# Kernel tuning notes

Measured on AMD Instinct MI355X. Metric: run time of the kernel, lower is better.

The kernel has to match this reference:

```python
import jax, jax.numpy as jnp
import numpy as np

HDIM = 1024
N_CLASSES = 50257
CUTOFFS = [2000, 10000, N_CLASSES]  # shortlist=2000, clusters: [2000,10000), [10000,50257)
DIV = 4.0
HEAD_SIZE = CUTOFFS[0] + 2  # shortlist + 2 cluster logits


def setup_inputs() -> dict:
    key = jax.random.key(0)
    ks = jax.random.split(key, 12)
    B, S, K = 8, 512, 256
    N = B * K
    hsz0 = int(HDIM // (DIV ** 1))  # 256
    hsz1 = int(HDIM // (DIV ** 2))  # 64
    osz0 = CUTOFFS[1] - CUTOFFS[0]  # 8000
    osz1 = CUTOFFS[2] - CUTOFFS[1]  # 40257
    w = 0.02
    return {
        "targets": jax.random.randint(ks[0], (N,), 0, N_CLASSES),
        "last_hidden_states": jax.random.normal(ks[1], (B, S, HDIM), dtype=jnp.float32),
        "cls_tokens_batch": jax.random.normal(ks[2], (B, HDIM), dtype=jnp.float32),
        "idx": jax.random.randint(ks[3], (B, K), 0, S),
        "head_W": jax.random.normal(ks[4], (HEAD_SIZE, HDIM), dtype=jnp.float32) * w,
        "head_b": jnp.zeros((HEAD_SIZE,), dtype=jnp.float32),
        "proj0_W": jax.random.normal(ks[5], (hsz0, HDIM), dtype=jnp.float32) * w,
        "out0_W": jax.random.normal(ks[6], (osz0, hsz0), dtype=jnp.float32) * w,
        "proj1_W": jax.random.normal(ks[7], (hsz1, HDIM), dtype=jnp.float32) * w,
        "out1_W": jax.random.normal(ks[8], (osz1, hsz1), dtype=jnp.float32) * w,
    }


def reference(targets, last_hidden_states, cls_tokens_batch, idx,
              head_W, head_b, proj0_W, out0_W, proj1_W, out1_W):
    # Gather context token embeddings: [B, K, H] -> [N, H]
    B, S, H = last_hidden_states.shape
    x = last_hidden_states[jnp.arange(B)[:, None], idx].reshape(-1, H)
    N = x.shape[0]
    c0, c1 = CUTOFFS[0], CUTOFFS[1]

    # Head: shortlist logits + per-cluster routing logits, [N, c0+2]
    head_logprob = jax.nn.log_softmax(x @ head_W.T + head_b, axis=-1)
    # Tail clusters: low-rank projection then output GEMM + log-softmax
    lp0 = jax.nn.log_softmax((x @ proj0_W.T) @ out0_W.T, axis=-1)  # [N, 8000]
    lp1 = jax.nn.log_softmax((x @ proj1_W.T) @ out1_W.T, axis=-1)  # [N, 40257]

    n = jnp.arange(N)
    t = targets
    short = head_logprob[n, jnp.clip(t, 0, c0 - 1)]
    mid = head_logprob[:, c0] + lp0[n, jnp.clip(t - c0, 0, lp0.shape[1] - 1)]
    high = head_logprob[:, c0 + 1] + lp1[n, jnp.clip(t - c1, 0, lp1.shape[1] - 1)]
    out = jnp.where(t < c0, short, jnp.where(t < c1, mid, high))  # target log-probs [N]
    loss = -jnp.mean(out)
    return out, loss
```

## Files before the change

### kernel.cpp

```cpp
#include <hip/hip_runtime.h>
#include <hip/hip_bf16.h>

#define NROWS 2048
#define L2E 1.4426950408889634f

typedef float f32x4 __attribute__((ext_vector_type(4)));
typedef __bf16 bf16x8 __attribute__((ext_vector_type(8)));
typedef short s16x8 __attribute__((ext_vector_type(8)));

typedef const __attribute__((address_space(1))) unsigned int* gas_t;
typedef __attribute__((address_space(3))) unsigned int* las_t;

__device__ __forceinline__ unsigned short f2bf(float f) {
    unsigned int u = __float_as_uint(f);
    unsigned int r = (u + 0x7FFFu + ((u >> 16) & 1u)) >> 16;
    return (unsigned short)r;
}
__device__ __forceinline__ float bf2f(unsigned short u) {
    return __uint_as_float((unsigned int)u << 16);
}
__device__ __forceinline__ f32x4 mfma16(s16x8 a, s16x8 b, f32x4 c) {
    return __builtin_amdgcn_mfma_f32_16x16x32_bf16(
        __builtin_bit_cast(bf16x8, a), __builtin_bit_cast(bf16x8, b), c, 0, 0, 0);
}

__global__ void k_prologue(const float* __restrict__ lhs, const int* __restrict__ idx,
                           const float* __restrict__ hw, const float* __restrict__ p0w,
                           const float* __restrict__ p1w, const float* __restrict__ o0w,
                           const float* __restrict__ o1w, const float* __restrict__ hb,
                           const int* __restrict__ tgt,
                           unsigned short* __restrict__ xb, unsigned short* __restrict__ hWb,
                           unsigned short* __restrict__ pW01, unsigned short* __restrict__ o0Wb,
                           unsigned short* __restrict__ o1Wb,
                           float* __restrict__ bias_s, int* __restrict__ tc) {
    int bid = blockIdx.x;
    if (bid < 2048) {
        int tid = bid * 256 + threadIdx.x;
        int n = tid >> 8;
        int c = (tid & 255) << 2;
        int b = n >> 8, k = n & 255;
        int srow = idx[(b << 8) + k];
        const float4 v = *reinterpret_cast<const float4*>(
            lhs + (((size_t)b << 9) + srow) * 1024 + c);
        ushort4 o = make_ushort4(f2bf(v.x), f2bf(v.y), f2bf(v.z), f2bf(v.w));
        *reinterpret_cast<ushort4*>(xb + (size_t)n * 1024 + c) = o;
        return;
    }
    bid -= 2048;
    if (bid < 6968) {
        const long B0 = 2048L * 1024;
        const long B1 = B0 + 384L * 1024;
        const long B2 = B1 + 8064L * 256;
        const long B3 = B2 + 40320L * 64;
        long e = ((long)bid * 256 + threadIdx.x) * 4;
        if (e >= B3) return;
        const float* src; unsigned short* dst; long rows; int colshift; long base;
        float sc;
        if (e < B0)      { base = 0;  src = hw;  dst = hWb;  rows = 2002;  colshift = 10; sc = L2E; }
        else if (e < B1) {
            long l = e - B0;
            long row = l >> 10;
            unsigned short* d = pW01 + l;
            ushort4 o;
            if (row < 256) {
                float4 v = *reinterpret_cast<const float4*>(p0w + l);
                o = make_ushort4(f2bf(v.x), f2bf(v.y), f2bf(v.z), f2bf(v.w));
            } else if (row < 320) {
                float4 v = *reinterpret_cast<const float4*>(p1w + (l - 256L * 1024));
                o = make_ushort4(f2bf(v.x), f2bf(v.y), f2bf(v.z), f2bf(v.w));
            } else {
                o = make_ushort4(0, 0, 0, 0);
            }
            *reinterpret_cast<ushort4*>(d) = o;
            return;
        }
        else if (e < B2) { base = B1; src = o0w; dst = o0Wb; rows = 8000;  colshift = 8; sc = L2E; }
        else             { base = B2; src = o1w; dst = o1Wb; rows = 40257; colshift = 6; sc = L2E; }
        long l = e - base;
        long row = l >> colshift;
        ushort4 o;
        if (row < rows) {
            float4 v = *reinterpret_cast<const float4*>(src + l);
            o = make_ushort4(f2bf(v.x * sc), f2bf(v.y * sc), f2bf(v.z * sc), f2bf(v.w * sc));
        } else {
            o = make_ushort4(0, 0, 0, 0);
        }
        *reinterpret_cast<ushort4*>(dst + l) = o;
        return;
    }
    bid -= 6968;
    int n = bid * 256 + threadIdx.x;
    if (n >= 2048) return;
    bias_s[n] = (n < 2002) ? hb[n] * L2E : -1e30f;
    int t = tgt[n];
    tc[n] = min(t, 1999);
    tc[2048 + n] = min(max(t - 2000, 0), 7999);
    tc[4096 + n] = min(max(t - 10000, 0), 40256);
}

template <int NT>
__global__ __launch_bounds__(256)
void k_mm(const unsigned short* __restrict__ A, int lda,
          const unsigned short* __restrict__ B, int ldb,
          const float* __restrict__ bias, float* __restrict__ partial,
          unsigned short* __restrict__ hout, int hstride, int hcols, int fsplit) {
    __shared__ unsigned short As[2][128 * 64];
    __shared__ unsigned short Bs[2][128 * 64];
    const int tid = threadIdx.x;
    const int lane = tid & 63, wid = tid >> 6;
    const int wr = wid >> 1, wc = wid & 1;
    const int g = lane >> 4, cl = lane & 15;
    const int row0 = blockIdx.x * 128;
    const int col0 = blockIdx.y * 128;

    const int sr = wid * 8 + (lane >> 3);
    const int swz = ((lane & 7) ^ (lane >> 3)) * 8;
    const unsigned short* Ab = A + (size_t)(row0 + sr) * lda + swz;
    const unsigned short* Bb = B + (size_t)(col0 + sr) * ldb + swz;

    auto stage = [&](int buf, int kt) {
        const unsigned short* ga = Ab + kt;
        const unsigned short* gb = Bb + kt;
        unsigned short* la = &As[buf][wid * 8 * 64];
        unsigned short* lb = &Bs[buf][wid * 8 * 64];
#pragma unroll
        for (int i = 0; i < 4; ++i) {
            __builtin_amdgcn_global_load_lds((gas_t)(const void*)(ga + (size_t)i * 32 * lda),
                                             (las_t)(void*)(la + i * 32 * 64), 16, 0, 0);
            __builtin_amdgcn_global_load_lds((gas_t)(const void*)(gb + (size_t)i * 32 * ldb),
                                             (las_t)(void*)(lb + i * 32 * 64), 16, 0, 0);
        }
    };

    f32x4 acc[4][4] = {};
    stage(0, 0);
    asm volatile("s_waitcnt vmcnt(0)" ::: "memory");
    __builtin_amdgcn_s_barrier();
    const int sA = (cl & 7);
    for (int t = 0; t < NT; ++t) {
        if (t + 1 < NT) stage((t + 1) & 1, (t + 1) * 64);
        const unsigned short* Al = &As[t & 1][(wr * 64 + cl) * 64];
        const unsigned short* Bl = &Bs[t & 1][(wc * 64 + cl) * 64];
#pragma unroll
        for (int kk2 = 0; kk2 < 2; ++kk2) {
            const int slot = ((kk2 * 4 + g) ^ sA) * 8;
            s16x8 a[4], b[4];
#pragma unroll
            for (int mi = 0; mi < 4; ++mi)
                a[mi] = *reinterpret_cast<const s16x8*>(Al + mi * 16 * 64 + slot);
#pragma unroll
            for (int ni = 0; ni < 4; ++ni)
                b[ni] = *reinterpret_cast<const s16x8*>(Bl + ni * 16 * 64 + slot);
#pragma unroll
            for (int mi = 0; mi < 4; ++mi)
#pragma unroll
                for (int ni = 0; ni < 4; ++ni)
                    acc[mi][ni] = mfma16(a[mi], b[ni], acc[mi][ni]);
        }
        if (t + 1 < NT) {
            asm volatile("s_waitcnt vmcnt(0)" ::: "memory");
            __builtin_amdgcn_s_barrier();
        }
    }

    if ((int)blockIdx.y >= fsplit) {
        int c0 = col0 - fsplit * 128;
#pragma unroll
        for (int mi = 0; mi < 4; ++mi)
#pragma unroll
            for (int ni = 0; ni < 4; ++ni) {
                int col = c0 + wc * 64 + ni * 16 + cl;
                if (col < hcols) {
#pragma unroll
                    for (int r = 0; r < 4; ++r) {
                        int row = row0 + wr * 64 + mi * 16 + g * 4 + r;
                        hout[(size_t)row * hstride + col] = f2bf(acc[mi][ni][r]);
                    }
                }
            }
    } else {
        float bv[4];
#pragma unroll
        for (int ni = 0; ni < 4; ++ni)
            bv[ni] = bias ? bias[col0 + wc * 64 + ni * 16 + cl] : 0.f;
        int strip = blockIdx.y * 2 + wc;
#pragma unroll
        for (int mi = 0; mi < 4; ++mi)
#pragma unroll
            for (int r = 0; r < 4; ++r) {
                float s = 0.f;
#pragma unroll
                for (int ni = 0; ni < 4; ++ni)
                    s += __builtin_amdgcn_exp2f(acc[mi][ni][r] + bv[ni]);
                s += __shfl_xor(s, 1, 64);
                s += __shfl_xor(s, 2, 64);
                s += __shfl_xor(s, 4, 64);
                s += __shfl_xor(s, 8, 64);
                if (cl == 0)
                    partial[(size_t)strip * NROWS + row0 + wr * 64 + mi * 16 + g * 4 + r] = s;
            }
    }
}

#define OUT1_IT 5
__global__ __launch_bounds__(256)
void k_tail(const unsigned short* __restrict__ h01, const unsigned short* __restrict__ o0Wb,
            const unsigned short* __restrict__ o1Wb, const unsigned short* __restrict__ xb,
            const float* __restrict__ headW, const float* __restrict__ hb,
            const float* __restrict__ o0w, const float* __restrict__ o1w,
            const int* __restrict__ tc,
            float* __restrict__ p0, float* __restrict__ p1,
            float* __restrict__ tgh, float* __restrict__ r0, float* __restrict__ r1,
            float* __restrict__ tg0, float* __restrict__ tg1) {
    __shared__ unsigned short smem[4][128 * 64];
    const int tid = threadIdx.x;
    const int lane = tid & 63, wid = tid >> 6;
    const int wr = wid >> 1, wc = wid & 1;
    const int g = lane >> 4, cl = lane & 15;
    int bid = blockIdx.x;

    if (bid < 1008) {
        const int row0 = (bid & 15) * 128;
        const int col0 = (bid >> 4) * 128;
        const int sr = wid * 8 + (lane >> 3);
        const int swz = ((lane & 7) ^ (lane >> 3)) * 8;
        const unsigned short* Ab = h01 + (size_t)(row0 + sr) * 320 + swz;
        const unsigned short* Bb = o0Wb + (size_t)(col0 + sr) * 256 + swz;
        auto stage = [&](int buf, int kt) {
            const unsigned short* ga = Ab + kt;
            const unsigned short* gb = Bb + kt;
            unsigned short* la = &smem[buf][wid * 8 * 64];
            unsigned short* lb = &smem[2 + buf][wid * 8 * 64];
#pragma unroll
            for (int i = 0; i < 4; ++i) {
                __builtin_amdgcn_global_load_lds((gas_t)(const void*)(ga + (size_t)i * 32 * 320),
                                                 (las_t)(void*)(la + i * 32 * 64), 16, 0, 0);
                __builtin_amdgcn_global_load_lds((gas_t)(const void*)(gb + (size_t)i * 32 * 256),
                                                 (las_t)(void*)(lb + i * 32 * 64), 16, 0, 0);
            }
        };
        f32x4 acc[4][4] = {};
        stage(0, 0);
        asm volatile("s_waitcnt vmcnt(0)" ::: "memory");
        __builtin_amdgcn_s_barrier();
        const int sA = (cl & 7);
        for (int t = 0; t < 4; ++t) {
            if (t < 3) stage((t + 1) & 1, (t + 1) * 64);
            const unsigned short* Al = &smem[t & 1][(wr * 64 + cl) * 64];
            const unsigned short* Bl = &smem[2 + (t & 1)][(wc * 64 + cl) * 64];
#pragma unroll
            for (int kk2 = 0; kk2 < 2; ++kk2) {
                const int slot = ((kk2 * 4 + g) ^ sA) * 8;
                s16x8 a[4], b[4];
#pragma unroll
                for (int mi = 0; mi < 4; ++mi)
                    a[mi] = *reinterpret_cast<const s16x8*>(Al + mi * 16 * 64 + slot);
#pragma unroll
                for (int ni = 0; ni < 4; ++ni)
                    b[ni] = *reinterpret_cast<const s16x8*>(Bl + ni * 16 * 64 + slot);
#pragma unroll
                for (int mi = 0; mi < 4; ++mi)
#pragma unroll
                    for (int ni = 0; ni < 4; ++ni)
                        acc[mi][ni] = mfma16(a[mi], b[ni], acc[mi][ni]);
            }
            if (t < 3) {
                asm volatile("s_waitcnt vmcnt(0)" ::: "memory");
                __builtin_amdgcn_s_barrier();
            }
        }
        int strip = (bid >> 4) * 2 + wc;
#pragma unroll
        for (int mi = 0; mi < 4; ++mi)
#pragma unroll
            for (int r = 0; r < 4; ++r) {
                float s = 0.f;
#pragma unroll
                for (int ni = 0; ni < 4; ++ni)
                    s += __builtin_amdgcn_exp2f(acc[mi][ni][r]);
                s += __shfl_xor(s, 1, 64);
                s += __shfl_xor(s, 2, 64);
                s += __shfl_xor(s, 4, 64);
                s += __shfl_xor(s, 8, 64);
                if (cl == 0)
                    p0[(size_t)strip * NROWS + row0 + wr * 64 + mi * 16 + g * 4 + r] = s;
            }
        return;
    }
    if (bid < 2016) {
        bid -= 1008;
        const int row0 = (bid & 15) * 128 + wr * 64;
        const int yb = bid >> 4;
        const int t0 = yb * OUT1_IT;
        s16x8 a[4][2];
#pragma unroll
        for (int mi = 0; mi < 4; ++mi)
#pragma unroll
            for (int kk = 0; kk < 2; ++kk)
                a[mi][kk] = *reinterpret_cast<const s16x8*>(
                    h01 + (size_t)(row0 + mi * 16 + cl) * 320 + 256 + kk * 32 + g * 8);
        const int sr = wid * 8 + (lane >> 3);
        const int swz = ((lane & 7) ^ (lane >> 3)) * 8;
        auto stage = [&](int buf, int tile) {
            const unsigned short* gb = o1Wb + ((size_t)tile * 128 + sr) * 64 + swz;
            unsigned short* lb = &smem[buf][wid * 8 * 64];
#pragma unroll
            for (int i = 0; i < 4; ++i)
                __builtin_amdgcn_global_load_lds((gas_t)(const void*)(gb + (size_t)i * 32 * 64),
                                                 (las_t)(void*)(lb + i * 32 * 64), 16, 0, 0);
        };
        float sexp[4][4] = {};
        const f32x4 z4 = {0.f, 0.f, 0.f, 0.f};
        stage(0, t0);
        asm volatile("s_waitcnt vmcnt(0)" ::: "memory");
        __builtin_amdgcn_s_barrier();
        int buf = 0;
        const int sA = (cl & 7);
#pragma unroll 1
        for (int it = 0; it < OUT1_IT; ++it) {
            if (it + 1 < OUT1_IT) stage(buf ^ 1, t0 + it + 1);
            const unsigned short* Bl = smem[buf];
#pragma unroll
            for (int ni = 0; ni < 4; ++ni) {
                const unsigned short* br = Bl + (wc * 64 + ni * 16 + cl) * 64;
                s16x8 b0 = *reinterpret_cast<const s16x8*>(br + (g ^ sA) * 8);
                s16x8 b1 = *reinterpret_cast<const s16x8*>(br + ((4 + g) ^ sA) * 8);
                f32x4 acc[4];
#pragma unroll
                for (int mi = 0; mi < 4; ++mi)
                    acc[mi] = mfma16(a[mi][0], b0, z4);
#pragma unroll
                for (int mi = 0; mi < 4; ++mi)
                    acc[mi] = mfma16(a[mi][1], b1, acc[mi]);
#pragma unroll
                for (int mi = 0; mi < 4; ++mi)
#pragma unroll
                    for (int r = 0; r < 4; ++r)
                        sexp[mi][r] += __builtin_amdgcn_exp2f(acc[mi][r]);
            }
            if (it + 1 < OUT1_IT) {
                asm volatile("s_waitcnt vmcnt(0)" ::: "memory");
                __builtin_amdgcn_s_barrier();
                buf ^= 1;
            }
        }
#pragma unroll
        for (int mi = 0; mi < 4; ++mi)
#pragma unroll
            for (int r = 0; r < 4; ++r) {
                float s = sexp[mi][r];
                s += __shfl_xor(s, 1, 64);
                s += __shfl_xor(s, 2, 64);
                s += __shfl_xor(s, 4, 64);
                s += __shfl_xor(s, 8, 64);
                if (cl == 0)
                    p1[(size_t)(yb * 2 + wc) * NROWS + row0 + mi * 16 + g * 4 + r] = s;
            }
        return;
    }
    bid -= 2016;
    int n = (bid * 256 + tid) >> 6;
    int tch = tc[n], tc0 = tc[2048 + n], tc1 = tc[4096 + n];
    const unsigned short* xr = xb + (size_t)n * 1024 + lane * 16;
    s16x8 x0 = *reinterpret_cast<const s16x8*>(xr);
    s16x8 x1 = *reinterpret_cast<const s16x8*>(xr + 8);
    const float* wh = headW + (size_t)tch * 1024 + lane * 16;
    const float* wa = headW + (size_t)2000 * 1024 + lane * 16;
    const float* wb = headW + (size_t)2001 * 1024 + lane * 16;
    float dh = 0.f, da = 0.f, db = 0.f;
#pragma unroll
    for (int i = 0; i < 8; ++i) {
        float xv = bf2f((unsigned short)x0[i]);
        dh += xv * wh[i]; da += xv * wa[i]; db += xv * wb[i];
    }
#pragma unroll
    for (int i = 0; i < 8; ++i) {
        float xv = bf2f((unsigned short)x1[i]);
        dh += xv * wh[8 + i]; da += xv * wa[8 + i]; db += xv * wb[8 + i];
    }
    ushort4 h0v = *reinterpret_cast<const ushort4*>(h01 + (size_t)n * 320 + lane * 4);
    float4 w0v = *reinterpret_cast<const float4*>(o0w + (size_t)tc0 * 256 + lane * 4);
    float d2 = bf2f(h0v.x) * w0v.x + bf2f(h0v.y) * w0v.y +
               bf2f(h0v.z) * w0v.z + bf2f(h0v.w) * w0v.w;
    float d3 = bf2f(h01[(size_t)n * 320 + 256 + lane]) * o1w[(size_t)tc1 * 64 + lane];
#pragma unroll
    for (int m = 1; m < 64; m <<= 1) {
        dh += __shfl_xor(dh, m, 64);
        da += __shfl_xor(da, m, 64);
        db += __shfl_xor(db, m, 64);
        d2 += __shfl_xor(d2, m, 64);
        d3 += __shfl_xor(d3, m, 64);
    }
    if (lane == 0) {
        tgh[n] = dh + hb[tch];
        r0[n] = da + hb[2000];
        r1[n] = db + hb[2001];
        tg0[n] = d2;
        tg1[n] = d3;
    }
}

__global__ void k_finalize(const float* __restrict__ ph, const float* __restrict__ p0,
                           const float* __restrict__ p1, const float* __restrict__ tgh,
                           const float* __restrict__ r0, const float* __restrict__ r1,
                           const float* __restrict__ tg0, const float* __restrict__ tg1,
                           const int* __restrict__ tgt, float* __restrict__ outv,
                           float* __restrict__ bsum) {
    int n = blockIdx.x * 128 + threadIdx.x;
    float sh = 0.f, s0 = 0.f, s1 = 0.f;
    for (int s = 0; s < 32; ++s) sh += ph[(size_t)s * NROWS + n];
    for (int s = 0; s < 126; ++s) s0 += p0[(size_t)s * NROWS + n];
    for (int s = 0; s < 126; ++s) s1 += p1[(size_t)s * NROWS + n];
    s0 -= 64.f;
    s1 -= 63.f;
    float lh = __logf(sh), l0 = __logf(s0), l1 = __logf(s1);
    int t = tgt[n];
    float o;
    if (t < 2000) o = tgh[n] - lh;
    else if (t < 10000) o = (r0[n] - lh) + (tg0[n] - l0);
    else o = (r1[n] - lh) + (tg1[n] - l1);
    outv[n] = o;
    __shared__ float red[128];
    red[threadIdx.x] = o;
    __syncthreads();
    for (int s = 64; s > 0; s >>= 1) {
        if (threadIdx.x < s) red[threadIdx.x] += red[threadIdx.x + s];
        __syncthreads();
    }
    if (threadIdx.x == 0) bsum[blockIdx.x] = red[0];
}

__global__ void k_loss(const float* __restrict__ bsum, float* __restrict__ loss) {
    float s = 0.f;
    for (int i = 0; i < 16; ++i) s += bsum[i];
    *loss = -s / (float)NROWS;
}

extern "C" void kernel_launch(void* const* d_in, const int* in_sizes, int n_in,
                              void* d_out, int out_size, void* d_ws, size_t ws_size,
                              hipStream_t stream) {
    const int* targets   = (const int*)d_in[0];
    const float* lhs     = (const float*)d_in[1];
    const int* idx       = (const int*)d_in[3];
    const float* head_W  = (const float*)d_in[4];
    const float* head_b  = (const float*)d_in[5];
    const float* proj0_W = (const float*)d_in[6];
    const float* out0_W  = (const float*)d_in[7];
    const float* proj1_W = (const float*)d_in[8];
    const float* out1_W  = (const float*)d_in[9];

    char* ws = (char*)d_ws;
    size_t off = 0;
    auto alloc = [&](size_t bytes) -> void* {
        void* p = ws + off;
        off += (bytes + 255) & ~(size_t)255;
        return p;
    };

    unsigned short* xb   = (unsigned short*)alloc((size_t)2048 * 1024 * 2);
    unsigned short* wB   = (unsigned short*)alloc((size_t)2432 * 1024 * 2);
    unsigned short* hWb  = wB;
    unsigned short* pW01 = wB + (size_t)2048 * 1024;
    unsigned short* o0Wb = (unsigned short*)alloc((size_t)8064 * 256 * 2);
    unsigned short* o1Wb = (unsigned short*)alloc((size_t)40320 * 64 * 2);
    unsigned short* h01  = (unsigned short*)alloc((size_t)2048 * 320 * 2);
    float* ph  = (float*)alloc((size_t)32 * 2048 * 4);
    float* p0  = (float*)alloc((size_t)126 * 2048 * 4);
    float* p1  = (float*)alloc((size_t)126 * 2048 * 4);
    float* tgh = (float*)alloc(2048 * 4);
    float* r0  = (float*)alloc(2048 * 4);
    float* r1  = (float*)alloc(2048 * 4);
    float* tg0 = (float*)alloc(2048 * 4);
    float* tg1 = (float*)alloc(2048 * 4);
    int*   tc  = (int*)alloc(3 * 2048 * 4);
    float* bias_s = (float*)alloc(2048 * 4);
    float* bsum = (float*)alloc(16 * 4);

    k_prologue<<<9024, 256, 0, stream>>>(lhs, idx, head_W, proj0_W, proj1_W, out0_W, out1_W,
                                         head_b, targets,
                                         xb, hWb, pW01, o0Wb, o1Wb, bias_s, tc);

    k_mm<16><<<dim3(16, 19), 256, 0, stream>>>(
        xb, 1024, wB, 1024, bias_s, ph, h01, 320, 320, 16);

    k_tail<<<2528, 256, 0, stream>>>(h01, o0Wb, o1Wb, xb, head_W, head_b, out0_W, out1_W,
                                     tc, p0, p1, tgh, r0, r1, tg0, tg1);

    float* outv = (float*)d_out;
    float* loss = (float*)d_out + NROWS;
    k_finalize<<<16, 128, 0, stream>>>(ph, p0, p1, tgh, r0, r1, tg0, tg1, targets, outv, bsum);
    k_loss<<<1, 1, 0, stream>>>(bsum, loss);
}
```

Baseline: 87.53 us.

## Compact rows by target cluster and skip tail GEMM tiles for absent rows

The prologue now builds per-cluster compacted row lists with a block-wide prefix scan over targets, recording the row count for each tail cluster. The tail GEMMs gather A rows through these lists and exit early for row tiles beyond the count, so only rows whose target falls in a cluster get that cluster's log-softmax denominator computed. Finalize reads the partial sums through the inverse index. With uniform random targets about 16% and 80% of rows land in the two clusters, so cluster 0 work shrinks a lot. The cost is a single-block serial scan in the prologue and indirect row loads.

```diff
diff --git a/kernel.cpp b/kernel.cpp
--- a/kernel.cpp
+++ b/kernel.cpp
@@ -32,7 +32,10 @@
                            unsigned short* __restrict__ xb, unsigned short* __restrict__ hWb,
                            unsigned short* __restrict__ pW01, unsigned short* __restrict__ o0Wb,
                            unsigned short* __restrict__ o1Wb,
-                           float* __restrict__ bias_s, int* __restrict__ tc) {
+                           float* __restrict__ bias_s, int* __restrict__ tc,
+                           int* __restrict__ rows0, int* __restrict__ rows1,
+                           int* __restrict__ idx0, int* __restrict__ idx1,
+                           int* __restrict__ cnt) {
     int bid = blockIdx.x;
     if (bid < 2048) {
         int tid = bid * 256 + threadIdx.x;
@@ -88,14 +91,42 @@
         *reinterpret_cast<ushort4*>(dst + l) = o;
         return;
     }
-    bid -= 6968;
-    int n = bid * 256 + threadIdx.x;
-    if (n >= 2048) return;
-    bias_s[n] = (n < 2002) ? hb[n] * L2E : -1e30f;
-    int t = tgt[n];
-    tc[n] = min(t, 1999);
-    tc[2048 + n] = min(max(t - 2000, 0), 7999);
-    tc[4096 + n] = min(max(t - 10000, 0), 40256);
+    __shared__ int sc0[256], sc1[256];
+    int t = threadIdx.x;
+    int myt[8];
+    int c0l = 0, c1l = 0;
+#pragma unroll
+    for (int i = 0; i < 8; ++i) {
+        int n = t * 8 + i;
+        int tt = tgt[n];
+        myt[i] = tt;
+        bias_s[n] = (n < 2002) ? hb[n] * L2E : -1e30f;
+        tc[n] = min(tt, 1999);
+        tc[2048 + n] = min(max(tt - 2000, 0), 7999);
+        tc[4096 + n] = min(max(tt - 10000, 0), 40256);
+        c0l += (tt >= 2000 && tt < 10000);
+        c1l += (tt >= 10000);
+    }
+    sc0[t] = c0l; sc1[t] = c1l;
+    __syncthreads();
+    for (int off = 1; off < 256; off <<= 1) {
+        int v0 = (t >= off) ? sc0[t - off] : 0;
+        int v1 = (t >= off) ? sc1[t - off] : 0;
+        __syncthreads();
+        sc0[t] += v0; sc1[t] += v1;
+        __syncthreads();
+    }
+    int p0pos = sc0[t] - c0l, p1pos = sc1[t] - c1l;
+#pragma unroll
+    for (int i = 0; i < 8; ++i) {
+        int n = t * 8 + i;
+        int tt = myt[i];
+        if (tt >= 2000 && tt < 10000) { rows0[p0pos] = n; idx0[n] = p0pos; ++p0pos; }
+        else idx0[n] = -1;
+        if (tt >= 10000) { rows1[p1pos] = n; idx1[n] = p1pos; ++p1pos; }
+        else idx1[n] = -1;
+    }
+    if (t == 255) { cnt[0] = sc0[255]; cnt[1] = sc1[255]; }
 }
 
 template <int NT>
@@ -209,6 +240,8 @@
             const float* __restrict__ headW, const float* __restrict__ hb,
             const float* __restrict__ o0w, const float* __restrict__ o1w,
             const int* __restrict__ tc,
+            const int* __restrict__ rows0, const int* __restrict__ rows1,
+            const int* __restrict__ cnt,
             float* __restrict__ p0, float* __restrict__ p1,
             float* __restrict__ tgh, float* __restrict__ r0, float* __restrict__ r1,
             float* __restrict__ tg0, float* __restrict__ tg1) {
@@ -220,22 +253,28 @@
     int bid = blockIdx.x;
 
     if (bid < 1008) {
-        const int row0 = (bid & 15) * 128;
+        const int c0n = cnt[0];
+        const int rt = bid & 15;
+        const int row0 = rt * 128;
+        if (row0 >= c0n) return;
         const int col0 = (bid >> 4) * 128;
         const int sr = wid * 8 + (lane >> 3);
         const int swz = ((lane & 7) ^ (lane >> 3)) * 8;
-        const unsigned short* Ab = h01 + (size_t)(row0 + sr) * 320 + swz;
+        const unsigned short* Arow[4];
+#pragma unroll
+        for (int i = 0; i < 4; ++i) {
+            int rp = min(row0 + sr + i * 32, c0n - 1);
+            Arow[i] = h01 + (size_t)rows0[rp] * 320 + swz;
+        }
         const unsigned short* Bb = o0Wb + (size_t)(col0 + sr) * 256 + swz;
         auto stage = [&](int buf, int kt) {
-            const unsigned short* ga = Ab + kt;
-            const unsigned short* gb = Bb + kt;
             unsigned short* la = &smem[buf][wid * 8 * 64];
             unsigned short* lb = &smem[2 + buf][wid * 8 * 64];
 #pragma unroll
             for (int i = 0; i < 4; ++i) {
-                __builtin_amdgcn_global_load_lds((gas_t)(const void*)(ga + (size_t)i * 32 * 320),
+                __builtin_amdgcn_global_load_lds((gas_t)(const void*)(Arow[i] + kt),
                                                  (las_t)(void*)(la + i * 32 * 64), 16, 0, 0);
-                __builtin_amdgcn_global_load_lds((gas_t)(const void*)(gb + (size_t)i * 32 * 256),
+                __builtin_amdgcn_global_load_lds((gas_t)(const void*)(Bb + kt + (size_t)i * 32 * 256),
                                                  (las_t)(void*)(lb + i * 32 * 64), 16, 0, 0);
             }
         };
@@ -289,16 +328,23 @@
     }
     if (bid < 2016) {
         bid -= 1008;
-        const int row0 = (bid & 15) * 128 + wr * 64;
+        const int c1n = cnt[1];
+        const int rt = bid & 15;
+        if (rt * 128 >= c1n) return;
+        const int row0c = rt * 128 + wr * 64;
         const int yb = bid >> 4;
         const int t0 = yb * OUT1_IT;
+        int grow[4];
+#pragma unroll
+        for (int mi = 0; mi < 4; ++mi)
+            grow[mi] = rows1[min(row0c + mi * 16 + cl, c1n - 1)];
         s16x8 a[4][2];
 #pragma unroll
         for (int mi = 0; mi < 4; ++mi)
 #pragma unroll
             for (int kk = 0; kk < 2; ++kk)
                 a[mi][kk] = *reinterpret_cast<const s16x8*>(
-                    h01 + (size_t)(row0 + mi * 16 + cl) * 320 + 256 + kk * 32 + g * 8);
+                    h01 + (size_t)grow[mi] * 320 + 256 + kk * 32 + g * 8);
         const int sr = wid * 8 + (lane >> 3);
         const int swz = ((lane & 7) ^ (lane >> 3)) * 8;
         auto stage = [&](int buf, int tile) {
@@ -354,7 +400,7 @@
                 s += __shfl_xor(s, 4, 64);
                 s += __shfl_xor(s, 8, 64);
                 if (cl == 0)
-                    p1[(size_t)(yb * 2 + wc) * NROWS + row0 + mi * 16 + g * 4 + r] = s;
+                    p1[(size_t)(yb * 2 + wc) * NROWS + row0c + mi * 16 + g * 4 + r] = s;
             }
         return;
     }
@@ -404,21 +450,30 @@
                            const float* __restrict__ p1, const float* __restrict__ tgh,
                            const float* __restrict__ r0, const float* __restrict__ r1,
                            const float* __restrict__ tg0, const float* __restrict__ tg1,
-                           const int* __restrict__ tgt, float* __restrict__ outv,
-                           float* __restrict__ bsum) {
+                           const int* __restrict__ tgt,
+                           const int* __restrict__ idx0, const int* __restrict__ idx1,
+                           float* __restrict__ outv, float* __restrict__ bsum) {
     int n = blockIdx.x * 128 + threadIdx.x;
-    float sh = 0.f, s0 = 0.f, s1 = 0.f;
+    float sh = 0.f;
     for (int s = 0; s < 32; ++s) sh += ph[(size_t)s * NROWS + n];
-    for (int s = 0; s < 126; ++s) s0 += p0[(size_t)s * NROWS + n];
-    for (int s = 0; s < 126; ++s) s1 += p1[(size_t)s * NROWS + n];
-    s0 -= 64.f;
-    s1 -= 63.f;
-    float lh = __logf(sh), l0 = __logf(s0), l1 = __logf(s1);
+    float lh = __logf(sh);
     int t = tgt[n];
     float o;
-    if (t < 2000) o = tgh[n] - lh;
-    else if (t < 10000) o = (r0[n] - lh) + (tg0[n] - l0);
-    else o = (r1[n] - lh) + (tg1[n] - l1);
+    if (t < 2000) {
+        o = tgh[n] - lh;
+    } else if (t < 10000) {
+        int ci = idx0[n];
+        float s0 = 0.f;
+        for (int s = 0; s < 126; ++s) s0 += p0[(size_t)s * NROWS + ci];
+        s0 -= 64.f;
+        o = (r0[n] - lh) + (tg0[n] - __logf(s0));
+    } else {
+        int ci = idx1[n];
+        float s1 = 0.f;
+        for (int s = 0; s < 126; ++s) s1 += p1[(size_t)s * NROWS + ci];
+        s1 -= 63.f;
+        o = (r1[n] - lh) + (tg1[n] - __logf(s1));
+    }
     outv[n] = o;
     __shared__ float red[128];
     red[threadIdx.x] = o;
@@ -474,20 +529,28 @@
     float* tg1 = (float*)alloc(2048 * 4);
     int*   tc  = (int*)alloc(3 * 2048 * 4);
     float* bias_s = (float*)alloc(2048 * 4);
+    int* rows0 = (int*)alloc(2048 * 4);
+    int* rows1 = (int*)alloc(2048 * 4);
+    int* idx0  = (int*)alloc(2048 * 4);
+    int* idx1  = (int*)alloc(2048 * 4);
+    int* cnt   = (int*)alloc(2 * 4);
     float* bsum = (float*)alloc(16 * 4);
 
-    k_prologue<<<9024, 256, 0, stream>>>(lhs, idx, head_W, proj0_W, proj1_W, out0_W, out1_W,
+    k_prologue<<<9017, 256, 0, stream>>>(lhs, idx, head_W, proj0_W, proj1_W, out0_W, out1_W,
                                          head_b, targets,
-                                         xb, hWb, pW01, o0Wb, o1Wb, bias_s, tc);
+                                         xb, hWb, pW01, o0Wb, o1Wb, bias_s, tc,
+                                         rows0, rows1, idx0, idx1, cnt);
 
     k_mm<16><<<dim3(16, 19), 256, 0, stream>>>(
         xb, 1024, wB, 1024, bias_s, ph, h01, 320, 320, 16);
 
     k_tail<<<2528, 256, 0, stream>>>(h01, o0Wb, o1Wb, xb, head_W, head_b, out0_W, out1_W,
-                                     tc, p0, p1, tgh, r0, r1, tg0, tg1);
+                                     tc, rows0, rows1, cnt, p0, p1,
+                                     tgh, r0, r1, tg0, tg1);
 
     float* outv = (float*)d_out;
     float* loss = (float*)d_out + NROWS;
-    k_finalize<<<16, 128, 0, stream>>>(ph, p0, p1, tgh, r0, r1, tg0, tg1, targets, outv, bsum);
+    k_finalize<<<16, 128, 0, stream>>>(ph, p0, p1, tgh, r0, r1, tg0, tg1, targets,
+                                       idx0, idx1, outv, bsum);
     k_loss<<<1, 1, 0, stream>>>(bsum, loss);
 }
```

Measured after the change: 93.37 us. +6.7%, slower.

## Halve head GEMM row tile for more blocks and fuse loss via atomic ticket

Applied to the files above, without the earlier changes.

The head/projection GEMM moves from 128x128 tiles to 64x128 tiles, with each of the four waves owning a 32-column strip. This doubles the grid to 32x19 blocks so more CUs are busy, and it doubles the number of softmax partial strips the finalize kernel sums. The separate single-thread loss kernel is removed: each finalize block adds its sum into a fixed-point 64-bit atomic accumulator, and the last block (found with a ticket counter) writes the loss. That saves one launch, but B tiles are re-read more often and the loss now depends on atomics and fixed-point rounding.

```diff
diff --git a/kernel.cpp b/kernel.cpp
--- a/kernel.cpp
+++ b/kernel.cpp
@@ -32,7 +32,9 @@
                            unsigned short* __restrict__ xb, unsigned short* __restrict__ hWb,
                            unsigned short* __restrict__ pW01, unsigned short* __restrict__ o0Wb,
                            unsigned short* __restrict__ o1Wb,
-                           float* __restrict__ bias_s, int* __restrict__ tc) {
+                           float* __restrict__ bias_s, int* __restrict__ tc,
+                           unsigned long long* __restrict__ lossacc,
+                           unsigned int* __restrict__ ticket) {
     int bid = blockIdx.x;
     if (bid < 2048) {
         int tid = bid * 256 + threadIdx.x;
@@ -91,6 +93,7 @@
     bid -= 6968;
     int n = bid * 256 + threadIdx.x;
     if (n >= 2048) return;
+    if (n == 0) { *lossacc = 0ull; *ticket = 0u; }
     bias_s[n] = (n < 2002) ? hb[n] * L2E : -1e30f;
     int t = tgt[n];
     tc[n] = min(t, 1999);
@@ -104,13 +107,13 @@
           const unsigned short* __restrict__ B, int ldb,
           const float* __restrict__ bias, float* __restrict__ partial,
           unsigned short* __restrict__ hout, int hstride, int hcols, int fsplit) {
-    __shared__ unsigned short As[2][128 * 64];
+    __shared__ unsigned short As[2][64 * 64];
     __shared__ unsigned short Bs[2][128 * 64];
     const int tid = threadIdx.x;
     const int lane = tid & 63, wid = tid >> 6;
-    const int wr = wid >> 1, wc = wid & 1;
+    const int wc = wid;
     const int g = lane >> 4, cl = lane & 15;
-    const int row0 = blockIdx.x * 128;
+    const int row0 = blockIdx.x * 64;
     const int col0 = blockIdx.y * 128;
 
     const int sr = wid * 8 + (lane >> 3);
@@ -119,42 +122,41 @@
     const unsigned short* Bb = B + (size_t)(col0 + sr) * ldb + swz;
 
     auto stage = [&](int buf, int kt) {
-        const unsigned short* ga = Ab + kt;
-        const unsigned short* gb = Bb + kt;
         unsigned short* la = &As[buf][wid * 8 * 64];
         unsigned short* lb = &Bs[buf][wid * 8 * 64];
 #pragma unroll
-        for (int i = 0; i < 4; ++i) {
-            __builtin_amdgcn_global_load_lds((gas_t)(const void*)(ga + (size_t)i * 32 * lda),
+        for (int i = 0; i < 2; ++i)
+            __builtin_amdgcn_global_load_lds((gas_t)(const void*)(Ab + kt + (size_t)i * 32 * lda),
                                              (las_t)(void*)(la + i * 32 * 64), 16, 0, 0);
-            __builtin_amdgcn_global_load_lds((gas_t)(const void*)(gb + (size_t)i * 32 * ldb),
+#pragma unroll
+        for (int i = 0; i < 4; ++i)
+            __builtin_amdgcn_global_load_lds((gas_t)(const void*)(Bb + kt + (size_t)i * 32 * ldb),
                                              (las_t)(void*)(lb + i * 32 * 64), 16, 0, 0);
-        }
     };
 
-    f32x4 acc[4][4] = {};
+    f32x4 acc[4][2] = {};
     stage(0, 0);
     asm volatile("s_waitcnt vmcnt(0)" ::: "memory");
     __builtin_amdgcn_s_barrier();
     const int sA = (cl & 7);
     for (int t = 0; t < NT; ++t) {
         if (t + 1 < NT) stage((t + 1) & 1, (t + 1) * 64);
-        const unsigned short* Al = &As[t & 1][(wr * 64 + cl) * 64];
-        const unsigned short* Bl = &Bs[t & 1][(wc * 64 + cl) * 64];
+        const unsigned short* Al = &As[t & 1][cl * 64];
+        const unsigned short* Bl = &Bs[t & 1][(wc * 32 + cl) * 64];
 #pragma unroll
         for (int kk2 = 0; kk2 < 2; ++kk2) {
             const int slot = ((kk2 * 4 + g) ^ sA) * 8;
-            s16x8 a[4], b[4];
+            s16x8 a[4], b[2];
 #pragma unroll
             for (int mi = 0; mi < 4; ++mi)
                 a[mi] = *reinterpret_cast<const s16x8*>(Al + mi * 16 * 64 + slot);
 #pragma unroll
-            for (int ni = 0; ni < 4; ++ni)
+            for (int ni = 0; ni < 2; ++ni)
                 b[ni] = *reinterpret_cast<const s16x8*>(Bl + ni * 16 * 64 + slot);
 #pragma unroll
             for (int mi = 0; mi < 4; ++mi)
 #pragma unroll
-                for (int ni = 0; ni < 4; ++ni)
+                for (int ni = 0; ni < 2; ++ni)
                     acc[mi][ni] = mfma16(a[mi], b[ni], acc[mi][ni]);
         }
         if (t + 1 < NT) {
@@ -168,36 +170,32 @@
 #pragma unroll
         for (int mi = 0; mi < 4; ++mi)
 #pragma unroll
-            for (int ni = 0; ni < 4; ++ni) {
-                int col = c0 + wc * 64 + ni * 16 + cl;
+            for (int ni = 0; ni < 2; ++ni) {
+                int col = c0 + wc * 32 + ni * 16 + cl;
                 if (col < hcols) {
 #pragma unroll
                     for (int r = 0; r < 4; ++r) {
-                        int row = row0 + wr * 64 + mi * 16 + g * 4 + r;
+                        int row = row0 + mi * 16 + g * 4 + r;
                         hout[(size_t)row * hstride + col] = f2bf(acc[mi][ni][r]);
                     }
                 }
             }
     } else {
-        float bv[4];
-#pragma unroll
-        for (int ni = 0; ni < 4; ++ni)
-            bv[ni] = bias ? bias[col0 + wc * 64 + ni * 16 + cl] : 0.f;
-        int strip = blockIdx.y * 2 + wc;
+        float bv0 = bias[col0 + wc * 32 + cl];
+        float bv1 = bias[col0 + wc * 32 + 16 + cl];
+        int strip = blockIdx.y * 4 + wc;
 #pragma unroll
         for (int mi = 0; mi < 4; ++mi)
 #pragma unroll
             for (int r = 0; r < 4; ++r) {
-                float s = 0.f;
-#pragma unroll
-                for (int ni = 0; ni < 4; ++ni)
-                    s += __builtin_amdgcn_exp2f(acc[mi][ni][r] + bv[ni]);
+                float s = __builtin_amdgcn_exp2f(acc[mi][0][r] + bv0)
+                        + __builtin_amdgcn_exp2f(acc[mi][1][r] + bv1);
                 s += __shfl_xor(s, 1, 64);
                 s += __shfl_xor(s, 2, 64);
                 s += __shfl_xor(s, 4, 64);
                 s += __shfl_xor(s, 8, 64);
                 if (cl == 0)
-                    partial[(size_t)strip * NROWS + row0 + wr * 64 + mi * 16 + g * 4 + r] = s;
+                    partial[(size_t)strip * NROWS + row0 + mi * 16 + g * 4 + r] = s;
             }
     }
 }
@@ -227,15 +225,13 @@
         const unsigned short* Ab = h01 + (size_t)(row0 + sr) * 320 + swz;
         const unsigned short* Bb = o0Wb + (size_t)(col0 + sr) * 256 + swz;
         auto stage = [&](int buf, int kt) {
-            const unsigned short* ga = Ab + kt;
-            const unsigned short* gb = Bb + kt;
             unsigned short* la = &smem[buf][wid * 8 * 64];
             unsigned short* lb = &smem[2 + buf][wid * 8 * 64];
 #pragma unroll
             for (int i = 0; i < 4; ++i) {
-                __builtin_amdgcn_global_load_lds((gas_t)(const void*)(ga + (size_t)i * 32 * 320),
+                __builtin_amdgcn_global_load_lds((gas_t)(const void*)(Ab + kt + (size_t)i * 32 * 320),
                                                  (las_t)(void*)(la + i * 32 * 64), 16, 0, 0);
-                __builtin_amdgcn_global_load_lds((gas_t)(const void*)(gb + (size_t)i * 32 * 256),
+                __builtin_amdgcn_global_load_lds((gas_t)(const void*)(Bb + kt + (size_t)i * 32 * 256),
                                                  (las_t)(void*)(lb + i * 32 * 64), 16, 0, 0);
             }
         };
@@ -405,10 +401,11 @@
                            const float* __restrict__ r0, const float* __restrict__ r1,
                            const float* __restrict__ tg0, const float* __restrict__ tg1,
                            const int* __restrict__ tgt, float* __restrict__ outv,
-                           float* __restrict__ bsum) {
+                           unsigned long long* __restrict__ lossacc,
+                           unsigned int* __restrict__ ticket) {
     int n = blockIdx.x * 128 + threadIdx.x;
     float sh = 0.f, s0 = 0.f, s1 = 0.f;
-    for (int s = 0; s < 32; ++s) sh += ph[(size_t)s * NROWS + n];
+    for (int s = 0; s < 64; ++s) sh += ph[(size_t)s * NROWS + n];
     for (int s = 0; s < 126; ++s) s0 += p0[(size_t)s * NROWS + n];
     for (int s = 0; s < 126; ++s) s1 += p1[(size_t)s * NROWS + n];
     s0 -= 64.f;
@@ -427,13 +424,17 @@
         if (threadIdx.x < s) red[threadIdx.x] += red[threadIdx.x + s];
         __syncthreads();
     }
-    if (threadIdx.x == 0) bsum[blockIdx.x] = red[0];
-}
-
-__global__ void k_loss(const float* __restrict__ bsum, float* __restrict__ loss) {
-    float s = 0.f;
-    for (int i = 0; i < 16; ++i) s += bsum[i];
-    *loss = -s / (float)NROWS;
+    if (threadIdx.x == 0) {
+        long long fx = __double2ll_rn((double)red[0] * 1048576.0);
+        atomicAdd(lossacc, (unsigned long long)fx);
+        __threadfence();
+        unsigned int tk = atomicAdd(ticket, 1u);
+        if (tk == 15u) {
+            unsigned long long v = atomicAdd(lossacc, 0ull);
+            long long sv = (long long)v;
+            outv[NROWS] = (float)(-((double)sv / 1048576.0) / 2048.0);
+        }
+    }
 }
 
 extern "C" void kernel_launch(void* const* d_in, const int* in_sizes, int n_in,
@@ -464,7 +465,7 @@
     unsigned short* o0Wb = (unsigned short*)alloc((size_t)8064 * 256 * 2);
     unsigned short* o1Wb = (unsigned short*)alloc((size_t)40320 * 64 * 2);
     unsigned short* h01  = (unsigned short*)alloc((size_t)2048 * 320 * 2);
-    float* ph  = (float*)alloc((size_t)32 * 2048 * 4);
+    float* ph  = (float*)alloc((size_t)64 * 2048 * 4);
     float* p0  = (float*)alloc((size_t)126 * 2048 * 4);
     float* p1  = (float*)alloc((size_t)126 * 2048 * 4);
     float* tgh = (float*)alloc(2048 * 4);
@@ -474,20 +475,21 @@
     float* tg1 = (float*)alloc(2048 * 4);
     int*   tc  = (int*)alloc(3 * 2048 * 4);
     float* bias_s = (float*)alloc(2048 * 4);
-    float* bsum = (float*)alloc(16 * 4);
+    unsigned long long* lossacc = (unsigned long long*)alloc(8);
+    unsigned int* ticket = (unsigned int*)alloc(4);
 
     k_prologue<<<9024, 256, 0, stream>>>(lhs, idx, head_W, proj0_W, proj1_W, out0_W, out1_W,
                                          head_b, targets,
-                                         xb, hWb, pW01, o0Wb, o1Wb, bias_s, tc);
-
-    k_mm<16><<<dim3(16, 19), 256, 0, stream>>>(
+                                         xb, hWb, pW01, o0Wb, o1Wb, bias_s, tc,
+                                         lossacc, ticket);
+
+    k_mm<16><<<dim3(32, 19), 256, 0, stream>>>(
         xb, 1024, wB, 1024, bias_s, ph, h01, 320, 320, 16);
 
     k_tail<<<2528, 256, 0, stream>>>(h01, o0Wb, o1Wb, xb, head_W, head_b, out0_W, out1_W,
                                      tc, p0, p1, tgh, r0, r1, tg0, tg1);
 
     float* outv = (float*)d_out;
-    float* loss = (float*)d_out + NROWS;
-    k_finalize<<<16, 128, 0, stream>>>(ph, p0, p1, tgh, r0, r1, tg0, tg1, targets, outv, bsum);
-    k_loss<<<1, 1, 0, stream>>>(bsum, loss);
-}
+    k_finalize<<<16, 128, 0, stream>>>(ph, p0, p1, tgh, r0, r1, tg0, tg1, targets,
+                                       outv, lossacc, ticket);
+}
```

After: 87.51 us, median of 2. No clear change (-0.0%).
